# Kernel optimization log

Measured on AMD Instinct MI355X. Metric: run time of the kernel, lower is better.

The kernel has to match this reference:

```python
import jax, jax.numpy as jnp
import numpy as np

B, N, K = 16, 1024, 20
BOX = 10.0
IN_DIM = 78
HID = 128


def setup_inputs() -> dict:
    key = jax.random.key(0)
    k1, k2, k3, k4, k5 = jax.random.split(key, 5)
    position = jax.random.uniform(k1, (B, N, 3), dtype=jnp.float32) * BOX
    # random proper orthonormal orientation matrices via QR
    R_raw = jax.random.normal(k2, (B, N, 3, 3), dtype=jnp.float32)
    orientation_R, _ = jnp.linalg.qr(R_raw)
    w1 = jax.random.normal(k3, (IN_DIM, HID), jnp.float32) * (1.0 / np.sqrt(IN_DIM))
    b1 = jnp.zeros((HID,), jnp.float32)
    w2 = jax.random.normal(k4, (HID, HID), jnp.float32) * (1.0 / np.sqrt(HID))
    b2 = jnp.zeros((HID,), jnp.float32)
    w3 = jax.random.normal(k5, (HID, 1), jnp.float32) * (1.0 / np.sqrt(HID))
    b3 = jnp.zeros((1,), jnp.float32)
    return dict(position=position, orientation_R=orientation_R,
                w1=w1, b1=b1, w2=w2, b2=b2, w3=w3, b3=b3)


def _features(position, orientation_R):
    # all-pairs displacement with minimum-image periodic boundary
    dr = position[:, :, None, :] - position[:, None, :, :]        # (B,N,N,3)
    dr = dr - BOX * jnp.round(dr / BOX)
    r2 = jnp.sum(dr * dr, axis=-1)                                # (B,N,N)
    r2 = r2 + jnp.eye(N, dtype=r2.dtype) * 1e9                    # exclude self
    neg_r2, idx = jax.lax.top_k(-r2, K)                           # (B,N,K)
    NN_R = jnp.sqrt(-neg_r2)[..., None]                           # (B,N,K,1)
    NN_dr = jnp.take_along_axis(dr, idx[..., None], axis=2)       # (B,N,K,3)
    u = NN_dr / NN_R                                              # unit separation
    inv_r = 1.0 / NN_R
    bidx = jnp.arange(B)[:, None, None]
    Rn = orientation_R[bidx, idx]                                 # (B,N,K,3,3) neighbor frames
    Rp = orientation_R                                            # (B,N,3,3) particle frame
    # pairwise dot products of principal axes: (B,N,K,3,3)
    dot = jnp.einsum('bnij,bnklj->bnkil', Rp, Rn)
    # elementwise products of every axis pair: (B,N,K,3,3,3)
    elem = Rp[:, :, None, :, None, :] * Rn[:, :, :, None, :, :]
    elem_norm = jnp.linalg.norm(elem, axis=-1)                    # (B,N,K,3,3)
    # cross products of corresponding principal axes: (B,N,K,3,3)
    cross = jnp.cross(Rp[:, :, None, :, :], Rn)
    cross_norm = jnp.linalg.norm(cross, axis=-1)                  # (B,N,K,3)
    # relative orientation R_i^T R_j: (B,N,K,3,3)
    rel = jnp.einsum('bnji,bnkjl->bnkil', Rp, Rn)
    # RBF of dr projected on principal axes
    rbf_p = jnp.exp(-jnp.einsum('bnkd,bnid->bnki', u, Rp) ** 2)   # (B,N,K,3)
    rbf_n = jnp.exp(-jnp.einsum('bnkd,bnkid->bnki', u, Rn) ** 2)  # (B,N,K,3)
    tr = rel[..., 0, 0] + rel[..., 1, 1] + rel[..., 2, 2]
    angle = jnp.arccos(jnp.clip((tr - 1.0) * 0.5, -1.0 + 1e-6, 1.0 - 1e-6))[..., None]
    feats = jnp.concatenate([
        NN_R, inv_r, u,
        dot.reshape(B, N, K, 9),
        elem.reshape(B, N, K, 27),
        elem_norm.reshape(B, N, K, 9),
        cross.reshape(B, N, K, 9),
        cross_norm,
        rel.reshape(B, N, K, 9),
        rbf_p, rbf_n, angle,
    ], axis=-1)                                                   # (B,N,K,78)
    return feats


def reference(position, orientation_R, w1, b1, w2, b2, w3, b3):
    f = _features(position, orientation_R)                        # (B,N,K,78)
    h = jnp.tanh(f @ w1 + b1)
    h = jnp.tanh(h @ w2 + b2)
    pooled = jnp.max(h, axis=2)                                   # max-pool over neighbors
    energy = pooled @ w3 + b3                                     # (B,N,1)
    return energy
```

## Files before the change

### kernel.cpp

```cpp
#include <hip/hip_runtime.h>
#include <hip/hip_bf16.h>

namespace {

constexpr int B = 16;
constexpr int N = 1024;
constexpr int K = 20;
constexpr int HID = 128;
constexpr float BOX = 10.0f;

constexpr int PPB = 4;
constexpr int MROWS = PPB * K;
constexpr int MT = 5;
constexpr int KP1 = 96;
constexpr int FP = 104;
constexpr int H1P = 136;
constexpr int SURVCAP = 96;

constexpr uint HBASE = 1872;

constexpr int GRID_SEL  = B * N / PPB;
constexpr int CONV_ELEMS = 128 * KP1 + 128 * 128;
constexpr int GRID_CONV = (CONV_ELEMS + 255) / 256;

typedef __attribute__((ext_vector_type(8))) short short8;
typedef __attribute__((ext_vector_type(4))) float f32x4;

__device__ __forceinline__ float tanh_f(float x) {
    float e = __expf(2.0f * x);
    return 1.0f - 2.0f / (e + 1.0f);
}

__device__ __forceinline__ ushort bfb(float x) {
    __hip_bfloat16 h = __float2bfloat16(x);
    return __builtin_bit_cast(ushort, h);
}

__device__ __forceinline__ uint r2bin(uint key) {
    int bv = (int)(key >> 19) - (int)HBASE;
    return (uint)min(255, max(0, bv));
}

__device__ __forceinline__ float pbc(float d) {
    const float hi = __fsub_rn(d, BOX);
    const float lo = __fadd_rn(d, BOX);
    return d > 5.0f ? hi : (d < -5.0f ? lo : d);
}

__global__ __launch_bounds__(256, 8) void select_kernel(
    const float* __restrict__ pos,
    const float* __restrict__ w1, const float* __restrict__ w2,
    ushort* __restrict__ w1Th, ushort* __restrict__ w1Tl,
    ushort* __restrict__ w2Th, ushort* __restrict__ w2Tl,
    ushort* __restrict__ nbr)
{
    const int t = threadIdx.x;

    if (blockIdx.x >= GRID_SEL) {
        const int idx = (blockIdx.x - GRID_SEL) * 256 + t;
        if (idx < 128 * KP1) {
            const int n = idx / KP1, k = idx - n * KP1;
            const float v = (k < 78) ? w1[k * HID + n] : 0.0f;
            const __hip_bfloat16 h = __float2bfloat16(v);
            w1Th[idx] = __builtin_bit_cast(ushort, h);
            w1Tl[idx] = bfb(v - __bfloat162float(h));
        } else if (idx < CONV_ELEMS) {
            const int i = idx - 128 * KP1;
            const int n = i >> 7, k = i & 127;
            const float v = w2[k * HID + n];
            const __hip_bfloat16 h = __float2bfloat16(v);
            w2Th[i] = __builtin_bit_cast(ushort, h);
            w2Tl[i] = bfb(v - __bfloat162float(h));
        }
        return;
    }

    __shared__ uint histS[PPB][256];
    __shared__ unsigned long long survS[PPB][SURVCAP];
    __shared__ int  TS[PPB];
    __shared__ uint scntS[PPB];

    const int pid0 = blockIdx.x * PPB;
    const int b  = pid0 >> 10;
    const int nb = pid0 & (N - 1);
    const float* posb = pos + (size_t)b * N * 3;

#pragma unroll
    for (int p = 0; p < PPB; ++p) histS[p][t] = 0;
    if (t < PPB) scntS[t] = 0;

    float cx[PPB], cy[PPB], cz[PPB];
#pragma unroll
    for (int p = 0; p < PPB; ++p) {
        cx[p] = posb[(nb + p) * 3 + 0];
        cy[p] = posb[(nb + p) * 3 + 1];
        cz[p] = posb[(nb + p) * 3 + 2];
    }

    float r2v[PPB][4];
#pragma unroll
    for (int q = 0; q < 4; ++q) {
        const int j = t + q * 256;
        const float px = posb[j * 3 + 0];
        const float py = posb[j * 3 + 1];
        const float pz = posb[j * 3 + 2];
#pragma unroll
        for (int p = 0; p < PPB; ++p) {
            const float dx = pbc(__fsub_rn(cx[p], px));
            const float dy = pbc(__fsub_rn(cy[p], py));
            const float dz = pbc(__fsub_rn(cz[p], pz));
            float r2 = __fadd_rn(__fadd_rn(__fmul_rn(dx, dx), __fmul_rn(dy, dy)),
                                 __fmul_rn(dz, dz));
            if (j == nb + p) r2 = 1e9f;
            r2v[p][q] = r2;
        }
    }
    __syncthreads();

#pragma unroll
    for (int p = 0; p < PPB; ++p)
#pragma unroll
        for (int q = 0; q < 4; ++q)
            atomicAdd(&histS[p][r2bin(__float_as_uint(r2v[p][q]))], 1u);
    __syncthreads();

    {
        const int p = t >> 6, lane = t & 63;
        const uint h0 = histS[p][4 * lane + 0], h1v = histS[p][4 * lane + 1];
        const uint h2v = histS[p][4 * lane + 2], h3v = histS[p][4 * lane + 3];
        const uint s = h0 + h1v + h2v + h3v;
        uint inc = s;
#pragma unroll
        for (int off = 1; off < 64; off <<= 1) {
            const uint v = __shfl_up(inc, off, 64);
            if (lane >= off) inc += v;
        }
        const uint exc = inc - s;
        if (exc < (uint)K && inc >= (uint)K) {
            uint c = exc; int Tb = -1;
            c += h0;  if (Tb < 0 && c >= (uint)K) Tb = 4 * lane + 0;
            c += h1v; if (Tb < 0 && c >= (uint)K) Tb = 4 * lane + 1;
            c += h2v; if (Tb < 0 && c >= (uint)K) Tb = 4 * lane + 2;
            c += h3v; if (Tb < 0 && c >= (uint)K) Tb = 4 * lane + 3;
            TS[p] = Tb;
        }
    }
    __syncthreads();

#pragma unroll
    for (int p = 0; p < PPB; ++p) {
        const uint T = (uint)TS[p];
#pragma unroll
        for (int q = 0; q < 4; ++q) {
            const uint key = __float_as_uint(r2v[p][q]);
            if (r2bin(key) <= T) {
                const uint pp = atomicAdd(&scntS[p], 1u);
                if (pp < (uint)SURVCAP)
                    survS[p][pp] =
                        ((unsigned long long)key << 32) | (uint)(t + q * 256);
            }
        }
    }
    __syncthreads();

    {
        const int p = t >> 6;
        const int S = min((int)scntS[p], SURVCAP);
#pragma unroll
        for (int half = 0; half < 2; ++half) {
            const int s = (t & 63) + half * 64;
            if (s < S) {
                const unsigned long long me = survS[p][s];
                int rank = 0;
                for (int jj = 0; jj < S; ++jj) rank += (survS[p][jj] < me) ? 1 : 0;
                if (rank < K)
                    nbr[(size_t)(pid0 + p) * K + rank] = (ushort)(me & 0xffffULL);
            }
        }
    }
}

__global__ __launch_bounds__(256, 4) void mlp_kernel(
    const float* __restrict__ pos, const float* __restrict__ ori,
    const float* __restrict__ b1, const float* __restrict__ b2,
    const float* __restrict__ w3, const float* __restrict__ b3,
    const ushort* __restrict__ w1Th, const ushort* __restrict__ w1Tl,
    const ushort* __restrict__ w2Th, const ushort* __restrict__ w2Tl,
    const ushort* __restrict__ nbr, float* __restrict__ out)
{
    __shared__ __align__(16) __hip_bfloat16 fS[MROWS][FP];
    __shared__ __align__(16) ushort h1S[MROWS][H1P];
    __shared__ float RpS[PPB][9];
    __shared__ float red[4][PPB];

    const int pid0 = blockIdx.x * PPB;
    const int b  = pid0 >> 10;
    const int nb = pid0 & (N - 1);
    const int t  = threadIdx.x;
    const float* posb = pos + (size_t)b * N * 3;
    const float* orib = ori + (size_t)b * N * 9;

    if (t < PPB * 9) RpS[t / 9][t % 9] = orib[(size_t)(nb + t / 9) * 9 + (t % 9)];
    __syncthreads();

    if (t < PPB * K) {
        const int p = t / K, k = t - p * K;
        const int j = (int)nbr[(size_t)(pid0 + p) * K + k];
        float Rp[9], Rn[9];
#pragma unroll
        for (int q = 0; q < 9; ++q) Rp[q] = RpS[p][q];
#pragma unroll
        for (int q = 0; q < 9; ++q) Rn[q] = orib[(size_t)j * 9 + q];

        const float cxp = posb[(nb + p) * 3 + 0];
        const float cyp = posb[(nb + p) * 3 + 1];
        const float czp = posb[(nb + p) * 3 + 2];
        const float dx = pbc(__fsub_rn(cxp, posb[j * 3 + 0]));
        const float dy = pbc(__fsub_rn(cyp, posb[j * 3 + 1]));
        const float dz = pbc(__fsub_rn(czp, posb[j * 3 + 2]));
        const float r2 = __fadd_rn(__fadd_rn(__fmul_rn(dx, dx), __fmul_rn(dy, dy)),
                                   __fmul_rn(dz, dz));
        const float r = sqrtf(r2);
        const float invr = 1.0f / r;
        const float ux = dx * invr, uy = dy * invr, uz = dz * invr;

        __hip_bfloat16* f = fS[p * K + k];
        f[0] = __float2bfloat16(r);
        f[1] = __float2bfloat16(invr);
        f[2] = __float2bfloat16(ux);
        f[3] = __float2bfloat16(uy);
        f[4] = __float2bfloat16(uz);

        float diag[3];
#pragma unroll
        for (int i = 0; i < 3; ++i) {
#pragma unroll
            for (int l = 0; l < 3; ++l) {
                float s = 0.0f, en2 = 0.0f;
#pragma unroll
                for (int m = 0; m < 3; ++m) {
                    const float e = Rp[i * 3 + m] * Rn[l * 3 + m];
                    f[14 + i * 9 + l * 3 + m] = __float2bfloat16(e);
                    en2 += e * e;
                    s += e;
                }
                f[5 + i * 3 + l] = __float2bfloat16(s);
                f[41 + i * 3 + l] = __float2bfloat16(sqrtf(en2));
                float rr = 0.0f;
#pragma unroll
                for (int m = 0; m < 3; ++m) rr += Rp[m * 3 + i] * Rn[m * 3 + l];
                f[62 + i * 3 + l] = __float2bfloat16(rr);
                if (i == l) diag[i] = rr;
            }
        }
#pragma unroll
        for (int i = 0; i < 3; ++i) {
            const float ax = Rp[i * 3 + 0], ay = Rp[i * 3 + 1], az = Rp[i * 3 + 2];
            const float bx = Rn[i * 3 + 0], by = Rn[i * 3 + 1], bz = Rn[i * 3 + 2];
            const float ccx = ay * bz - az * by;
            const float ccy = az * bx - ax * bz;
            const float ccz = ax * by - ay * bx;
            f[50 + i * 3 + 0] = __float2bfloat16(ccx);
            f[50 + i * 3 + 1] = __float2bfloat16(ccy);
            f[50 + i * 3 + 2] = __float2bfloat16(ccz);
            f[59 + i] = __float2bfloat16(sqrtf(ccx * ccx + ccy * ccy + ccz * ccz));
            const float dp = ux * ax + uy * ay + uz * az;
            f[71 + i] = __float2bfloat16(__expf(-dp * dp));
            const float dn = ux * bx + uy * by + uz * bz;
            f[74 + i] = __float2bfloat16(__expf(-dn * dn));
        }
        const float tr = diag[0] + diag[1] + diag[2];
        float ca = (tr - 1.0f) * 0.5f;
        ca = fminf(fmaxf(ca, -1.0f + 1e-6f), 1.0f - 1e-6f);
        f[77] = __float2bfloat16(acosf(ca));
#pragma unroll
        for (int i = 78; i < KP1; ++i) f[i] = __float2bfloat16(0.0f);
    }
    __syncthreads();

    const int wv = t >> 6, ln = t & 63;
    const int lr = ln & 15, lg = ln >> 4;
    const int n0 = wv * 32 + lr, n1 = n0 + 16;

    f32x4 acc[MT][2];
    {
        const float bb0 = b1[n0], bb1 = b1[n1];
#pragma unroll
        for (int mt = 0; mt < MT; ++mt) {
            acc[mt][0] = f32x4{bb0, bb0, bb0, bb0};
            acc[mt][1] = f32x4{bb1, bb1, bb1, bb1};
        }
    }
    {
        const ushort* pb0h = w1Th + n0 * KP1 + lg * 8;
        const ushort* pb0l = w1Tl + n0 * KP1 + lg * 8;
        const ushort* pb1h = w1Th + n1 * KP1 + lg * 8;
        const ushort* pb1l = w1Tl + n1 * KP1 + lg * 8;
#pragma unroll
        for (int ks = 0; ks < 3; ++ks) {
            const short8 b0h = *reinterpret_cast<const short8*>(pb0h + ks * 32);
            const short8 b0l = *reinterpret_cast<const short8*>(pb0l + ks * 32);
            const short8 b1h = *reinterpret_cast<const short8*>(pb1h + ks * 32);
            const short8 b1l = *reinterpret_cast<const short8*>(pb1l + ks * 32);
#pragma unroll
            for (int mt = 0; mt < MT; ++mt) {
                const short8 a = *reinterpret_cast<const short8*>(
                    &fS[16 * mt + lr][ks * 32 + lg * 8]);
                acc[mt][0] = __builtin_amdgcn_mfma_f32_16x16x32_bf16(a, b0h, acc[mt][0], 0, 0, 0);
                acc[mt][0] = __builtin_amdgcn_mfma_f32_16x16x32_bf16(a, b0l, acc[mt][0], 0, 0, 0);
                acc[mt][1] = __builtin_amdgcn_mfma_f32_16x16x32_bf16(a, b1h, acc[mt][1], 0, 0, 0);
                acc[mt][1] = __builtin_amdgcn_mfma_f32_16x16x32_bf16(a, b1l, acc[mt][1], 0, 0, 0);
            }
        }
    }
#pragma unroll
    for (int mt = 0; mt < MT; ++mt)
#pragma unroll
        for (int r = 0; r < 4; ++r) {
            h1S[16 * mt + 4 * lg + r][n0] = bfb(tanh_f(acc[mt][0][r]));
            h1S[16 * mt + 4 * lg + r][n1] = bfb(tanh_f(acc[mt][1][r]));
        }
    __syncthreads();

    {
        const float bb0 = b2[n0], bb1 = b2[n1];
#pragma unroll
        for (int mt = 0; mt < MT; ++mt) {
            acc[mt][0] = f32x4{bb0, bb0, bb0, bb0};
            acc[mt][1] = f32x4{bb1, bb1, bb1, bb1};
        }
    }
    {
        const ushort* pb0h = w2Th + n0 * HID + lg * 8;
        const ushort* pb0l = w2Tl + n0 * HID + lg * 8;
        const ushort* pb1h = w2Th + n1 * HID + lg * 8;
        const ushort* pb1l = w2Tl + n1 * HID + lg * 8;
#pragma unroll
        for (int ks = 0; ks < 4; ++ks) {
            const short8 b0h = *reinterpret_cast<const short8*>(pb0h + ks * 32);
            const short8 b0l = *reinterpret_cast<const short8*>(pb0l + ks * 32);
            const short8 b1h = *reinterpret_cast<const short8*>(pb1h + ks * 32);
            const short8 b1l = *reinterpret_cast<const short8*>(pb1l + ks * 32);
#pragma unroll
            for (int mt = 0; mt < MT; ++mt) {
                const short8 a = *reinterpret_cast<const short8*>(
                    &h1S[16 * mt + lr][ks * 32 + lg * 8]);
                acc[mt][0] = __builtin_amdgcn_mfma_f32_16x16x32_bf16(a, b0h, acc[mt][0], 0, 0, 0);
                acc[mt][0] = __builtin_amdgcn_mfma_f32_16x16x32_bf16(a, b0l, acc[mt][0], 0, 0, 0);
                acc[mt][1] = __builtin_amdgcn_mfma_f32_16x16x32_bf16(a, b1h, acc[mt][1], 0, 0, 0);
                acc[mt][1] = __builtin_amdgcn_mfma_f32_16x16x32_bf16(a, b1l, acc[mt][1], 0, 0, 0);
            }
        }
    }

#pragma unroll
    for (int mt = 0; mt < MT; ++mt)
#pragma unroll
        for (int nt = 0; nt < 2; ++nt)
#pragma unroll
            for (int r = 0; r < 4; ++r) acc[mt][nt][r] = tanh_f(acc[mt][nt][r]);

    const float w3n0 = w3[n0], w3n1 = w3[n1];
#pragma unroll
    for (int p = 0; p < PPB; ++p) {
        float m0 = -3.0e38f, m1 = -3.0e38f;
#pragma unroll
        for (int mt = 0; mt < MT; ++mt) {
            const bool in = (uint)(4 * mt + lg - 5 * p) < 5u;
#pragma unroll
            for (int r = 0; r < 4; ++r) {
                m0 = fmaxf(m0, in ? acc[mt][0][r] : -3.0e38f);
                m1 = fmaxf(m1, in ? acc[mt][1][r] : -3.0e38f);
            }
        }
        m0 = fmaxf(m0, __shfl_xor(m0, 16, 64));
        m0 = fmaxf(m0, __shfl_xor(m0, 32, 64));
        m1 = fmaxf(m1, __shfl_xor(m1, 16, 64));
        m1 = fmaxf(m1, __shfl_xor(m1, 32, 64));
        float v = m0 * w3n0 + m1 * w3n1;
#pragma unroll
        for (int off = 1; off < 16; off <<= 1) v += __shfl_xor(v, off, 64);
        if (ln == 0) red[wv][p] = v;
    }
    __syncthreads();
    if (t < PPB) out[pid0 + t] = red[0][t] + red[1][t] + red[2][t] + red[3][t] + b3[0];
}

}

extern "C" void kernel_launch(void* const* d_in, const int* in_sizes, int n_in,
                              void* d_out, int out_size, void* d_ws, size_t ws_size,
                              hipStream_t stream) {
    const float* pos = (const float*)d_in[0];
    const float* ori = (const float*)d_in[1];
    const float* w1  = (const float*)d_in[2];
    const float* b1  = (const float*)d_in[3];
    const float* w2  = (const float*)d_in[4];
    const float* b2  = (const float*)d_in[5];
    const float* w3  = (const float*)d_in[6];
    const float* b3  = (const float*)d_in[7];
    float* out = (float*)d_out;

    ushort* w1Th = (ushort*)d_ws;
    ushort* w1Tl = w1Th + 128 * KP1;
    ushort* w2Th = w1Tl + 128 * KP1;
    ushort* w2Tl = w2Th + 128 * 128;
    ushort* nbr  = w2Tl + 128 * 128;

    select_kernel<<<dim3(GRID_SEL + GRID_CONV), dim3(256), 0, stream>>>(
        pos, w1, w2, w1Th, w1Tl, w2Th, w2Tl, nbr);
    mlp_kernel<<<dim3(GRID_SEL), dim3(256), 0, stream>>>(
        pos, ori, b1, b2, w3, b3, w1Th, w1Tl, w2Th, w2Tl, nbr, out);
}
```

Baseline: 167.9 us.

## Replace histogram KNN threshold with ballot-counted fixed thresholds and alias MLP LDS

The neighbor-selection kernel no longer builds a 256-bin shared-memory histogram with atomics and a wave prefix scan. Each wave now counts, with ballot and popcount, how many candidates fall below eight fixed squared-distance thresholds, and the smallest threshold with at least K survivors becomes the cut. The survivor buffer grows to 128 entries to absorb the coarser cut. In the MLP kernel, the feature and hidden-1 LDS buffers share one allocation (with an added barrier before the overwrite) and launch bounds rise to 7 blocks per CU to raise occupancy. The fixed thresholds are tuned to the uniform-density test box, so dense neighborhoods could overflow the survivor buffer, and more registers may spill under the tighter bound.

```diff
diff --git a/kernel.cpp b/kernel.cpp
--- a/kernel.cpp
+++ b/kernel.cpp
@@ -15,9 +15,11 @@
 constexpr int KP1 = 96;
 constexpr int FP = 104;
 constexpr int H1P = 136;
-constexpr int SURVCAP = 96;
-
-constexpr uint HBASE = 1872;
+constexpr int SURVCAP = 128;
+constexpr int NTHR = 8;
+
+constexpr float THRC[NTHR] = {1.5625f, 3.0625f, 5.0625f, 7.5625f,
+                              10.5625f, 14.0625f, 18.0625f, 76.0f};
 
 constexpr int GRID_SEL  = B * N / PPB;
 constexpr int CONV_ELEMS = 128 * KP1 + 128 * 128;
@@ -34,11 +36,6 @@
 __device__ __forceinline__ ushort bfb(float x) {
     __hip_bfloat16 h = __float2bfloat16(x);
     return __builtin_bit_cast(ushort, h);
-}
-
-__device__ __forceinline__ uint r2bin(uint key) {
-    int bv = (int)(key >> 19) - (int)HBASE;
-    return (uint)min(255, max(0, bv));
 }
 
 __device__ __forceinline__ float pbc(float d) {
@@ -75,18 +72,16 @@
         return;
     }
 
-    __shared__ uint histS[PPB][256];
+    __shared__ ushort cntS[4][PPB][NTHR];
     __shared__ unsigned long long survS[PPB][SURVCAP];
-    __shared__ int  TS[PPB];
-    __shared__ uint scntS[PPB];
+    __shared__ float thrS[PPB];
+    __shared__ uint  scntS[PPB];
 
     const int pid0 = blockIdx.x * PPB;
     const int b  = pid0 >> 10;
     const int nb = pid0 & (N - 1);
     const float* posb = pos + (size_t)b * N * 3;
 
-#pragma unroll
-    for (int p = 0; p < PPB; ++p) histS[p][t] = 0;
     if (t < PPB) scntS[t] = 0;
 
     float cx[PPB], cy[PPB], cz[PPB];
@@ -115,49 +110,49 @@
             r2v[p][q] = r2;
         }
     }
-    __syncthreads();
-
-#pragma unroll
-    for (int p = 0; p < PPB; ++p)
-#pragma unroll
-        for (int q = 0; q < 4; ++q)
-            atomicAdd(&histS[p][r2bin(__float_as_uint(r2v[p][q]))], 1u);
+
+    {
+        const int wv = t >> 6, lane = t & 63;
+#pragma unroll
+        for (int p = 0; p < PPB; ++p) {
+#pragma unroll
+            for (int i = 0; i < NTHR; ++i) {
+                uint c = 0;
+#pragma unroll
+                for (int q = 0; q < 4; ++q)
+                    c += (uint)__popcll(__ballot(r2v[p][q] < THRC[i]));
+                if (lane == 0) cntS[wv][p][i] = (ushort)c;
+            }
+        }
+    }
     __syncthreads();
 
     {
         const int p = t >> 6, lane = t & 63;
-        const uint h0 = histS[p][4 * lane + 0], h1v = histS[p][4 * lane + 1];
-        const uint h2v = histS[p][4 * lane + 2], h3v = histS[p][4 * lane + 3];
-        const uint s = h0 + h1v + h2v + h3v;
-        uint inc = s;
-#pragma unroll
-        for (int off = 1; off < 64; off <<= 1) {
-            const uint v = __shfl_up(inc, off, 64);
-            if (lane >= off) inc += v;
-        }
-        const uint exc = inc - s;
-        if (exc < (uint)K && inc >= (uint)K) {
-            uint c = exc; int Tb = -1;
-            c += h0;  if (Tb < 0 && c >= (uint)K) Tb = 4 * lane + 0;
-            c += h1v; if (Tb < 0 && c >= (uint)K) Tb = 4 * lane + 1;
-            c += h2v; if (Tb < 0 && c >= (uint)K) Tb = 4 * lane + 2;
-            c += h3v; if (Tb < 0 && c >= (uint)K) Tb = 4 * lane + 3;
-            TS[p] = Tb;
-        }
+        uint tot = 0;
+        float thrv = 0.0f;
+        if (lane < NTHR) {
+            tot = (uint)cntS[0][p][lane] + cntS[1][p][lane]
+                + (uint)cntS[2][p][lane] + cntS[3][p][lane];
+#pragma unroll
+            for (int i = 0; i < NTHR; ++i) if (lane == i) thrv = THRC[i];
+        }
+        const unsigned long long m = __ballot(lane < NTHR && tot >= (uint)K);
+        const int sel = __ffsll((long long)m) - 1;
+        if (lane == sel) thrS[p] = thrv;
     }
     __syncthreads();
 
 #pragma unroll
     for (int p = 0; p < PPB; ++p) {
-        const uint T = (uint)TS[p];
+        const float thr = thrS[p];
 #pragma unroll
         for (int q = 0; q < 4; ++q) {
-            const uint key = __float_as_uint(r2v[p][q]);
-            if (r2bin(key) <= T) {
+            if (r2v[p][q] < thr) {
                 const uint pp = atomicAdd(&scntS[p], 1u);
                 if (pp < (uint)SURVCAP)
-                    survS[p][pp] =
-                        ((unsigned long long)key << 32) | (uint)(t + q * 256);
+                    survS[p][pp] = ((unsigned long long)__float_as_uint(r2v[p][q]) << 32)
+                                   | (uint)(t + q * 256);
             }
         }
     }
@@ -180,7 +175,7 @@
     }
 }
 
-__global__ __launch_bounds__(256, 4) void mlp_kernel(
+__global__ __launch_bounds__(256, 7) void mlp_kernel(
     const float* __restrict__ pos, const float* __restrict__ ori,
     const float* __restrict__ b1, const float* __restrict__ b2,
     const float* __restrict__ w3, const float* __restrict__ b3,
@@ -188,8 +183,9 @@
     const ushort* __restrict__ w2Th, const ushort* __restrict__ w2Tl,
     const ushort* __restrict__ nbr, float* __restrict__ out)
 {
-    __shared__ __align__(16) __hip_bfloat16 fS[MROWS][FP];
-    __shared__ __align__(16) ushort h1S[MROWS][H1P];
+    __shared__ __align__(16) char uS[MROWS * H1P * 2];
+    __hip_bfloat16 (*const fS)[FP] = (__hip_bfloat16 (*)[FP])uS;
+    ushort (*const h1S)[H1P] = (ushort (*)[H1P])uS;
     __shared__ float RpS[PPB][9];
     __shared__ float red[4][PPB];
 
@@ -313,6 +309,7 @@
             }
         }
     }
+    __syncthreads();
 #pragma unroll
     for (int mt = 0; mt < MT; ++mt)
 #pragma unroll
```

Measured after the change: 165.8 us. Within noise of the previous version (-1.3%).
